# Optimization experiments

Hardware: AMD Instinct MI355X
Metric: run time of the kernel (lower is better)

Reference implementation:

```python
import jax, jax.numpy as jnp
import numpy as np

E_DIM = 640   # RNA-FM embedding dim
H = 256       # hidden_dim
L = 3         # num_gcn_layers
LN_EPS = 1e-5


def _layer_norm(x, g, b):
    mu = jnp.mean(x, axis=-1, keepdims=True)
    var = jnp.mean((x - mu) ** 2, axis=-1, keepdims=True)
    return (x - mu) * jax.lax.rsqrt(var + LN_EPS) * g + b


def setup_inputs() -> dict:
    key = jax.random.key(0)
    ks = jax.random.split(key, 20)
    B, S = 4, 256

    def w(k, shape):
        fan_in = shape[-2] if len(shape) >= 2 else shape[-1]
        return jax.random.normal(k, shape, dtype=jnp.float32) / np.sqrt(fan_in)

    inp = {
        "embeddings": jax.random.normal(ks[0], (B, S, E_DIM), dtype=jnp.float32),
        "bp_priors": jax.random.uniform(ks[1], (B, S, S), dtype=jnp.float32),
        "sequence_lengths": jnp.full((B,), S, dtype=jnp.int32),
        # FeatureEncoder: Linear(640, 512) -> ReLU -> Linear(512, 256)
        "enc_w1": w(ks[2], (E_DIM, 2 * H)), "enc_b1": jnp.zeros((2 * H,), jnp.float32),
        "enc_w2": w(ks[3], (2 * H, H)),     "enc_b2": jnp.zeros((H,), jnp.float32),
        # GCN layers (stacked over L)
        "gcn_wself": w(ks[4], (L, H, H)), "gcn_bself": jnp.zeros((L, H), jnp.float32),
        "gcn_wedge": w(ks[5], (L, H, H)), "gcn_bedge": jnp.zeros((L, H), jnp.float32),
        "gcn_ln_g": jnp.ones((L, H), jnp.float32), "gcn_ln_b": jnp.zeros((L, H), jnp.float32),
        # PairwiseScorer MLP: Linear(2H+1, H) -> ReLU -> Linear(H, H//2) -> ReLU -> Linear(H//2, 1)
        "mlp_w1": w(ks[6], (2 * H + 1, H)), "mlp_b1": jnp.zeros((H,), jnp.float32),
        "mlp_w2": w(ks[7], (H, H // 2)),    "mlp_b2": jnp.zeros((H // 2,), jnp.float32),
        "mlp_w3": w(ks[8], (H // 2, 1)),    "mlp_b3": jnp.zeros((1,), jnp.float32),
    }
    return inp


def reference(embeddings, bp_priors, sequence_lengths,
              enc_w1, enc_b1, enc_w2, enc_b2,
              gcn_wself, gcn_bself, gcn_wedge, gcn_bedge, gcn_ln_g, gcn_ln_b,
              mlp_w1, mlp_b1, mlp_w2, mlp_b2, mlp_w3, mlp_b3):
    # FeatureEncoder
    h = jax.nn.relu(embeddings @ enc_w1 + enc_b1) @ enc_w2 + enc_b2  # [B,S,H]

    # GCN layers: self GEMM + adjacency (bp_priors) aggregated neighbor GEMM
    for l in range(L):
        self_f = h @ gcn_wself[l] + gcn_bself[l]
        neigh_f = jnp.einsum('bij,bjh->bih', bp_priors, h @ gcn_wedge[l] + gcn_bedge[l])
        h = _layer_norm(jax.nn.relu(self_f + neigh_f), gcn_ln_g[l], gcn_ln_b[l])

    # PairwiseScorer: concat([node_i, node_j, prior]) @ W1 split into three partial products
    # (mathematically identical to the expand-concat-MLP in the torch module).
    hi = h @ mlp_w1[:H]           # [B,S,H] contribution of node_i
    hj = h @ mlp_w1[H:2 * H]      # [B,S,H] contribution of node_j
    p = jax.nn.relu(hi[:, :, None, :] + hj[:, None, :, :]
                    + bp_priors[..., None] * mlp_w1[2 * H] + mlp_b1)  # [B,S,S,H]
    p = jax.nn.relu(p @ mlp_w2 + mlp_b2)                              # [B,S,S,H//2]
    bp_scores = (p @ mlp_w3 + mlp_b3)[..., 0]                         # [B,S,S]
    return bp_scores
```

## Files before the change

### kernel.cpp

```cpp
#include <hip/hip_runtime.h>

typedef __attribute__((ext_vector_type(8))) short short8;
typedef __attribute__((ext_vector_type(4))) float f32x4;

__device__ __forceinline__ void gload_lds16(const void* g, void* l) {
    __builtin_amdgcn_global_load_lds(
        (const __attribute__((address_space(1))) unsigned*)g,
        (__attribute__((address_space(3))) unsigned*)l, 16, 0, 0);
}
#define MFMA16(a, b, c) __builtin_amdgcn_mfma_f32_16x16x32_bf16((a), (b), (c), 0, 0, 0)

__global__ __launch_bounds__(256)
void splitw2(const float* __restrict__ w2, short* __restrict__ w2th,
             short* __restrict__ w2tl)
{
    int e = blockIdx.x * 256 + threadIdx.x;
    int k = e >> 7, n = e & 127;
    float x = w2[e];
    unsigned hu = __float_as_uint(x) & 0xFFFF0000u;
    w2th[n * 256 + k] = (short)(hu >> 16);
    w2tl[n * 256 + k] = (short)(__float_as_uint(x - __uint_as_float(hu)) >> 16);
}

template<bool RELU, bool LNA>
__global__ __launch_bounds__(256)
void gemm_f32(const float* __restrict__ A,
              const float* __restrict__ B0, const float* __restrict__ bias0,
              float* __restrict__ C0,
              const float* __restrict__ B1, const float* __restrict__ bias1,
              float* __restrict__ C1,
              const float* __restrict__ ps, const float* __restrict__ lg,
              const float* __restrict__ lb,
              int M, int N, int K, int nxHalf)
{
    int bx = blockIdx.x;
    const float* B = B0; const float* bias = bias0; float* C = C0;
    if (nxHalf && bx >= nxHalf) { bx -= nxHalf; B = B1; bias = bias1; C = C1; }
    const int m0 = blockIdx.y * 32, n0 = bx * 64;
    const int tid = threadIdx.x;
    const int tx = tid & 15, ty = tid >> 4;

    __shared__ __align__(16) float As[32 * 36];
    __shared__ __align__(16) float Bs[32 * 68];
    __shared__ float mus[32], rss[32];

    if (LNA) {
        if (tid < 32) {
            int m = m0 + tid;
            float s  = ps[m * 2]            + ps[2048 + m * 2]
                     + ps[4096 + m * 2]     + ps[6144 + m * 2];
            float s2 = ps[m * 2 + 1]        + ps[2048 + m * 2 + 1]
                     + ps[4096 + m * 2 + 1] + ps[6144 + m * 2 + 1];
            float mu  = s * (1.f / 256.f);
            float var = s2 * (1.f / 256.f) - mu * mu;
            mus[tid] = mu;
            rss[tid] = rsqrtf(var + 1e-5f);
        }
        __syncthreads();
    }

    float acc[2][4] = {};
    for (int k0 = 0; k0 < K; k0 += 32) {
        {
            int row = tid >> 3, kq = (tid & 7) << 2;
            float4 v = *(const float4*)&A[(long)(m0 + row) * K + k0 + kq];
            if (LNA) {
                float4 gv = *(const float4*)&lg[k0 + kq];
                float4 bv = *(const float4*)&lb[k0 + kq];
                float mu = mus[row], rs = rss[row];
                v.x = (v.x - mu) * rs * gv.x + bv.x;
                v.y = (v.y - mu) * rs * gv.y + bv.y;
                v.z = (v.z - mu) * rs * gv.z + bv.z;
                v.w = (v.w - mu) * rs * gv.w + bv.w;
            }
            As[(kq + 0) * 36 + row] = v.x; As[(kq + 1) * 36 + row] = v.y;
            As[(kq + 2) * 36 + row] = v.z; As[(kq + 3) * 36 + row] = v.w;
        }
#pragma unroll
        for (int q = 0; q < 2; ++q) {
            int f = tid * 2 + q;
            int kk = f >> 4, nn = (f & 15) << 2;
            *(float4*)&Bs[kk * 68 + nn] = *(const float4*)&B[(long)(k0 + kk) * N + n0 + nn];
        }
        __syncthreads();
#pragma unroll
        for (int k = 0; k < 32; ++k) {
            float2 a2 = *(const float2*)&As[k * 36 + ty * 2];
            float4 b4 = *(const float4*)&Bs[k * 68 + tx * 4];
            acc[0][0] += a2.x * b4.x; acc[0][1] += a2.x * b4.y;
            acc[0][2] += a2.x * b4.z; acc[0][3] += a2.x * b4.w;
            acc[1][0] += a2.y * b4.x; acc[1][1] += a2.y * b4.y;
            acc[1][2] += a2.y * b4.z; acc[1][3] += a2.y * b4.w;
        }
        __syncthreads();
    }

#pragma unroll
    for (int i = 0; i < 2; ++i) {
        int m = m0 + ty * 2 + i;
#pragma unroll
        for (int j = 0; j < 4; ++j) {
            int n = n0 + tx * 4 + j;
            float v = acc[i][j];
            if (bias) v += bias[n];
            if (RELU) v = fmaxf(v, 0.f);
            C[(long)m * N + n] = v;
        }
    }
}

__global__ __launch_bounds__(256)
void bmm_fuse(const float* __restrict__ bp, const float* __restrict__ eg,
              const float* __restrict__ sf, float* __restrict__ x,
              float* __restrict__ ps)
{
    const int b = blockIdx.z, jb = blockIdx.x;
    const int m0 = blockIdx.y * 32, n0 = jb * 64;
    const float* A = bp + b * 65536;
    const float* B = eg + b * 65536;
    const int tid = threadIdx.x;
    const int tx = tid & 15, ty = tid >> 4;

    __shared__ __align__(16) float As[32 * 36];
    __shared__ __align__(16) float Bs[32 * 68];

    float acc[2][4] = {};
    for (int k0 = 0; k0 < 256; k0 += 32) {
        {
            int row = tid >> 3, kq = (tid & 7) << 2;
            float4 v = *(const float4*)&A[(long)(m0 + row) * 256 + k0 + kq];
            As[(kq + 0) * 36 + row] = v.x; As[(kq + 1) * 36 + row] = v.y;
            As[(kq + 2) * 36 + row] = v.z; As[(kq + 3) * 36 + row] = v.w;
        }
#pragma unroll
        for (int q = 0; q < 2; ++q) {
            int f = tid * 2 + q;
            int kk = f >> 4, nn = (f & 15) << 2;
            *(float4*)&Bs[kk * 68 + nn] = *(const float4*)&B[(long)(k0 + kk) * 256 + n0 + nn];
        }
        __syncthreads();
#pragma unroll
        for (int k = 0; k < 32; ++k) {
            float2 a2 = *(const float2*)&As[k * 36 + ty * 2];
            float4 b4 = *(const float4*)&Bs[k * 68 + tx * 4];
            acc[0][0] += a2.x * b4.x; acc[0][1] += a2.x * b4.y;
            acc[0][2] += a2.x * b4.z; acc[0][3] += a2.x * b4.w;
            acc[1][0] += a2.y * b4.x; acc[1][1] += a2.y * b4.y;
            acc[1][2] += a2.y * b4.z; acc[1][3] += a2.y * b4.w;
        }
        __syncthreads();
    }

#pragma unroll
    for (int i = 0; i < 2; ++i) {
        int gm = b * 256 + m0 + ty * 2 + i;
        float s = 0.f, s2 = 0.f;
#pragma unroll
        for (int j = 0; j < 4; ++j) {
            int n = n0 + tx * 4 + j;
            float v = fmaxf(acc[i][j] + sf[(long)gm * 256 + n], 0.f);
            x[(long)gm * 256 + n] = v;
            s += v; s2 += v * v;
        }
        s  += __shfl_xor(s, 1, 64);  s2 += __shfl_xor(s2, 1, 64);
        s  += __shfl_xor(s, 2, 64);  s2 += __shfl_xor(s2, 2, 64);
        s  += __shfl_xor(s, 4, 64);  s2 += __shfl_xor(s2, 4, 64);
        s  += __shfl_xor(s, 8, 64);  s2 += __shfl_xor(s2, 8, 64);
        if (tx == 0) {
            ps[jb * 2048 + gm * 2]     = s;
            ps[jb * 2048 + gm * 2 + 1] = s2;
        }
    }
}

#define STAGE_HJ(T, BUF)                                                        \
    {                                                                           \
        int row = tid >> 3, q = tid & 7;                                        \
        gload_lds16(&hja[((long)(b * 256 + j0 + row)) * 256 + (T) * 32          \
                         + (q ^ (row & 7)) * 4],                                \
                    (char*)&hjs[BUF][0] + tid * 16);                            \
        int row2 = row + 32;                                                    \
        gload_lds16(&hja[((long)(b * 256 + j0 + row2)) * 256 + (T) * 32         \
                         + (q ^ (row2 & 7)) * 4],                               \
                    (char*)&hjs[BUF][0] + 4096 + tid * 16);                     \
    }

#define BUILD_P(KT, BUF)                                                        \
    {                                                                           \
        const int p = tid >> 1, kb = (tid & 1) << 4;                            \
        const int ii = p >> 6, jj = p & 63;                                     \
        const float bw = bpv[p];                                                \
        const int swz = (p & 7) << 4;                                           \
        char* ph = (char*)&Ph[BUF][0];                                          \
        char* pl = (char*)&Pl[BUF][0];                                          \
        const char* hbase = (const char*)&hjs[BUF][0] + jj * 128;               \
        _Pragma("unroll")                                                       \
        for (int q = 0; q < 4; ++q) {                                           \
            int kk = kb + q * 4;                                                \
            float4 hv = *(const float4*)(hbase + ((((kk >> 2) ^ (jj & 7))) << 4)); \
            float4 iv = *(const float4*)&hib[ii][(KT) * 32 + kk];               \
            float4 cv = *(const float4*)&csv[(KT) * 32 + kk];                   \
            float x0 = fmaxf(iv.x + hv.x + bw * cv.x, 0.f);                     \
            float x1 = fmaxf(iv.y + hv.y + bw * cv.y, 0.f);                     \
            float x2 = fmaxf(iv.z + hv.z + bw * cv.z, 0.f);                     \
            float x3 = fmaxf(iv.w + hv.w + bw * cv.w, 0.f);                     \
            unsigned h0 = __float_as_uint(x0) & 0xFFFF0000u;                    \
            unsigned h1 = __float_as_uint(x1) & 0xFFFF0000u;                    \
            unsigned h2 = __float_as_uint(x2) & 0xFFFF0000u;                    \
            unsigned h3 = __float_as_uint(x3) & 0xFFFF0000u;                    \
            unsigned l0 = __float_as_uint(x0 - __uint_as_float(h0));            \
            unsigned l1 = __float_as_uint(x1 - __uint_as_float(h1));            \
            unsigned l2 = __float_as_uint(x2 - __uint_as_float(h2));            \
            unsigned l3 = __float_as_uint(x3 - __uint_as_float(h3));            \
            int bb2 = p * 64 + kk * 2;                                          \
            *(unsigned*)(ph + ((bb2    ) ^ swz)) = (h0 >> 16) | h1;             \
            *(unsigned*)(ph + ((bb2 + 4) ^ swz)) = (h2 >> 16) | h3;             \
            *(unsigned*)(pl + ((bb2    ) ^ swz)) = (l0 >> 16) | (l1 & 0xFFFF0000u); \
            *(unsigned*)(pl + ((bb2 + 4) ^ swz)) = (l2 >> 16) | (l3 & 0xFFFF0000u); \
        }                                                                       \
    }

__global__ __launch_bounds__(256, 3)
void pairwise3(const float* __restrict__ hia, const float* __restrict__ hja,
               const float* __restrict__ bpm,
               const float* __restrict__ c, const float* __restrict__ b1,
               const short* __restrict__ w2th, const short* __restrict__ w2tl,
               const float* __restrict__ b2, const float* __restrict__ w3,
               const float* __restrict__ b3, float* __restrict__ out)
{
    const int b = blockIdx.z, ib0 = blockIdx.y * 2, j0 = blockIdx.x * 64;
    const int tid = threadIdx.x, l = tid & 63, wid = tid >> 6;
    const int wm0 = (wid & 1) * 64, wn0 = (wid >> 1) * 64;
    const int g = l >> 4, ln = l & 15;

    __shared__ __align__(16) short Ph[2][4096];
    __shared__ __align__(16) short Pl[2][4096];
    __shared__ __align__(16) float hjs[2][2048];
    __shared__ __align__(16) float hib[2][256];
    __shared__ __align__(16) float csv[256];
    __shared__ float bpv[128];
    __shared__ float red[128][2];

    if (tid < 128)
        bpv[tid] = bpm[((long)(b * 256 + ib0 + (tid >> 6))) * 256 + j0 + (tid & 63)];
    {
        int i2 = tid >> 7, kk = (tid & 127) * 2;
        float2 hv = *(const float2*)&hia[((long)(b * 256 + ib0 + i2)) * 256 + kk];
        float2 bv = *(const float2*)&b1[kk];
        hib[i2][kk] = hv.x + bv.x; hib[i2][kk + 1] = hv.y + bv.y;
    }
    if (tid < 64) *(float4*)&csv[tid * 4] = *(const float4*)&c[tid * 4];

    STAGE_HJ(0, 0);
    __syncthreads();
    STAGE_HJ(1, 1);
    BUILD_P(0, 0);
    __syncthreads();

    f32x4 acc[4][4] = {};

#pragma unroll
    for (int kt = 0; kt < 8; ++kt) {
        const int cur = kt & 1;
        short8 bh[4], bl[4];
#pragma unroll
        for (int nf = 0; nf < 4; ++nf) {
            int col = wn0 + nf * 16 + ln;
            long bo = (long)col * 256 + kt * 32 + g * 8;
            bh[nf] = *(const short8*)(w2th + bo);
            bl[nf] = *(const short8*)(w2tl + bo);
        }
        short8 ah[4], al[4];
#pragma unroll
        for (int mf = 0; mf < 4; ++mf) {
            int row = wm0 + mf * 16 + ln;
            int off = (row * 64 + g * 16) ^ ((row & 7) << 4);
            ah[mf] = *(const short8*)((const char*)&Ph[cur][0] + off);
            al[mf] = *(const short8*)((const char*)&Pl[cur][0] + off);
        }
        if (kt < 6) STAGE_HJ(kt + 2, cur);
        if (kt < 7) BUILD_P(kt + 1, cur ^ 1);
#pragma unroll
        for (int mf = 0; mf < 4; ++mf)
#pragma unroll
            for (int nf = 0; nf < 4; ++nf) {
                acc[mf][nf] = MFMA16(ah[mf], bh[nf], acc[mf][nf]);
                acc[mf][nf] = MFMA16(ah[mf], bl[nf], acc[mf][nf]);
                acc[mf][nf] = MFMA16(al[mf], bh[nf], acc[mf][nf]);
            }
        __syncthreads();
    }

    float b2v[4], w3v[4];
#pragma unroll
    for (int nf = 0; nf < 4; ++nf) {
        int col = wn0 + nf * 16 + ln;
        b2v[nf] = b2[col];
        w3v[nf] = w3[col];
    }
#pragma unroll
    for (int mf = 0; mf < 4; ++mf) {
#pragma unroll
        for (int r = 0; r < 4; ++r) {
            float s = 0.f;
#pragma unroll
            for (int nf = 0; nf < 4; ++nf)
                s += fmaxf(acc[mf][nf][r] + b2v[nf], 0.f) * w3v[nf];
            s += __shfl_xor(s, 1, 64);
            s += __shfl_xor(s, 2, 64);
            s += __shfl_xor(s, 4, 64);
            s += __shfl_xor(s, 8, 64);
            if (ln == 0)
                red[wm0 + mf * 16 + g * 4 + r][wid >> 1] = s;
        }
    }
    __syncthreads();
    if (tid < 128) {
        int i = ib0 + (tid >> 6), j = j0 + (tid & 63);
        out[((long)(b * 256 + i)) * 256 + j] = red[tid][0] + red[tid][1] + b3[0];
    }
}

extern "C" void kernel_launch(void* const* d_in, const int* in_sizes, int n_in,
                              void* d_out, int out_size, void* d_ws, size_t ws_size,
                              hipStream_t stream)
{
    const float* emb   = (const float*)d_in[0];
    const float* bp    = (const float*)d_in[1];
    const float* ew1   = (const float*)d_in[3];
    const float* eb1   = (const float*)d_in[4];
    const float* ew2   = (const float*)d_in[5];
    const float* eb2   = (const float*)d_in[6];
    const float* wself = (const float*)d_in[7];
    const float* bself = (const float*)d_in[8];
    const float* wedge = (const float*)d_in[9];
    const float* bedge = (const float*)d_in[10];
    const float* lng   = (const float*)d_in[11];
    const float* lnb   = (const float*)d_in[12];
    const float* mw1   = (const float*)d_in[13];
    const float* mb1   = (const float*)d_in[14];
    const float* mw2   = (const float*)d_in[15];
    const float* mb2   = (const float*)d_in[16];
    const float* mw3   = (const float*)d_in[17];
    const float* mb3   = (const float*)d_in[18];
    float* out = (float*)d_out;

    float* ws = (float*)d_ws;
    float* h1 = ws;
    float* xe = h1 + 524288;
    float* sf = xe + 262144;
    float* eg = sf + 262144;
    float* x0 = eg + 262144;
    float* x1 = x0 + 262144;
    float* x2 = x1 + 262144;
    float* hi = x2 + 262144;
    float* hj = hi + 262144;
    short* w2th = (short*)(hj + 262144);
    short* w2tl = w2th + 32768;
    float* ps0  = (float*)(w2tl + 32768);
    float* ps1  = ps0 + 8192;
    float* ps2  = ps1 + 8192;

    float* xs[3]  = {x0, x1, x2};
    float* pss[3] = {ps0, ps1, ps2};
    dim3 blk(256);

    splitw2<<<dim3(128), blk, 0, stream>>>(mw2, w2th, w2tl);

    gemm_f32<true, false><<<dim3(8, 32), blk, 0, stream>>>(emb, ew1, eb1, h1,
        nullptr, nullptr, nullptr, nullptr, nullptr, nullptr, 1024, 512, 640, 0);
    gemm_f32<false, false><<<dim3(4, 32), blk, 0, stream>>>(h1, ew2, eb2, xe,
        nullptr, nullptr, nullptr, nullptr, nullptr, nullptr, 1024, 256, 512, 0);

    for (int l = 0; l < 3; ++l) {
        const float* Ain = (l == 0) ? xe : xs[l - 1];
        if (l == 0)
            gemm_f32<false, false><<<dim3(8, 32), blk, 0, stream>>>(Ain,
                wself, bself, sf, wedge, bedge, eg,
                nullptr, nullptr, nullptr, 1024, 256, 256, 4);
        else
            gemm_f32<false, true><<<dim3(8, 32), blk, 0, stream>>>(Ain,
                wself + l * 65536, bself + l * 256, sf,
                wedge + l * 65536, bedge + l * 256, eg,
                pss[l - 1], lng + (l - 1) * 256, lnb + (l - 1) * 256,
                1024, 256, 256, 4);
        bmm_fuse<<<dim3(4, 8, 4), blk, 0, stream>>>(bp, eg, sf, xs[l], pss[l]);
    }

    gemm_f32<false, true><<<dim3(8, 32), blk, 0, stream>>>(x2,
        mw1, nullptr, hi, mw1 + 65536, nullptr, hj,
        ps2, lng + 512, lnb + 512, 1024, 256, 256, 4);

    pairwise3<<<dim3(4, 128, 4), blk, 0, stream>>>(hi, hj, bp,
        mw1 + 131072, mb1, w2th, w2tl, mb2, mw3, mb3, out);
}
```

Measured before the change: 315.6 us.

## Shrink GEMM tiles, fold w2 split into encoder GEMM, vectorize pairwise P build

The fp32 GEMM kernel drops from a 32x64 to a 32x32 output tile per block, doubling the grid so more CUs are busy on these small matrices. The standalone splitw2 launch is merged into the first encoder GEMM as extra blocks, removing one launch. In the pairwise kernel, BUILD_P now handles 8 contiguous k values per thread and writes 16-byte stores instead of four 4-byte stores. The STAGE_HJ/BUILD_P calls are moved ahead of the A-fragment LDS reads to change the overlap with the MFMAs. Smaller tiles cut per-thread reuse and raise load traffic per FLOP in the GEMMs.

```diff
diff --git a/kernel.cpp b/kernel.cpp
--- a/kernel.cpp
+++ b/kernel.cpp
@@ -2,6 +2,7 @@
 
 typedef __attribute__((ext_vector_type(8))) short short8;
 typedef __attribute__((ext_vector_type(4))) float f32x4;
+typedef __attribute__((ext_vector_type(4))) unsigned uint4v;
 
 __device__ __forceinline__ void gload_lds16(const void* g, void* l) {
     __builtin_amdgcn_global_load_lds(
@@ -10,38 +11,39 @@
 }
 #define MFMA16(a, b, c) __builtin_amdgcn_mfma_f32_16x16x32_bf16((a), (b), (c), 0, 0, 0)
 
+template<bool RELU, bool LNA, bool SPLITW2>
 __global__ __launch_bounds__(256)
-void splitw2(const float* __restrict__ w2, short* __restrict__ w2th,
-             short* __restrict__ w2tl)
+void gemm_s(const float* __restrict__ A,
+            const float* __restrict__ B0, const float* __restrict__ bias0,
+            float* __restrict__ C0,
+            const float* __restrict__ B1, const float* __restrict__ bias1,
+            float* __restrict__ C1,
+            const float* __restrict__ ps, const float* __restrict__ lg,
+            const float* __restrict__ lb,
+            int M, int N, int K, int nxHalf,
+            const float* __restrict__ w2, short* __restrict__ w2th,
+            short* __restrict__ w2tl)
 {
-    int e = blockIdx.x * 256 + threadIdx.x;
-    int k = e >> 7, n = e & 127;
-    float x = w2[e];
-    unsigned hu = __float_as_uint(x) & 0xFFFF0000u;
-    w2th[n * 256 + k] = (short)(hu >> 16);
-    w2tl[n * 256 + k] = (short)(__float_as_uint(x - __uint_as_float(hu)) >> 16);
-}
-
-template<bool RELU, bool LNA>
-__global__ __launch_bounds__(256)
-void gemm_f32(const float* __restrict__ A,
-              const float* __restrict__ B0, const float* __restrict__ bias0,
-              float* __restrict__ C0,
-              const float* __restrict__ B1, const float* __restrict__ bias1,
-              float* __restrict__ C1,
-              const float* __restrict__ ps, const float* __restrict__ lg,
-              const float* __restrict__ lb,
-              int M, int N, int K, int nxHalf)
-{
+    if (SPLITW2 && blockIdx.y >= 32) {
+        int e = ((blockIdx.y - 32) * gridDim.x + blockIdx.x) * 256 + threadIdx.x;
+        if (e < 32768) {
+            int k = e >> 7, n = e & 127;
+            float x = w2[e];
+            unsigned hu = __float_as_uint(x) & 0xFFFF0000u;
+            w2th[n * 256 + k] = (short)(hu >> 16);
+            w2tl[n * 256 + k] = (short)(__float_as_uint(x - __uint_as_float(hu)) >> 16);
+        }
+        return;
+    }
     int bx = blockIdx.x;
     const float* B = B0; const float* bias = bias0; float* C = C0;
     if (nxHalf && bx >= nxHalf) { bx -= nxHalf; B = B1; bias = bias1; C = C1; }
-    const int m0 = blockIdx.y * 32, n0 = bx * 64;
+    const int m0 = blockIdx.y * 32, n0 = bx * 32;
     const int tid = threadIdx.x;
-    const int tx = tid & 15, ty = tid >> 4;
+    const int tx = tid & 7, ty = tid >> 3;
 
     __shared__ __align__(16) float As[32 * 36];
-    __shared__ __align__(16) float Bs[32 * 68];
+    __shared__ __align__(16) float Bs[32 * 36];
     __shared__ float mus[32], rss[32];
 
     if (LNA) {
@@ -59,10 +61,10 @@
         __syncthreads();
     }
 
-    float acc[2][4] = {};
+    float acc[4] = {};
     for (int k0 = 0; k0 < K; k0 += 32) {
         {
-            int row = tid >> 3, kq = (tid & 7) << 2;
+            int row = ty, kq = tx << 2;
             float4 v = *(const float4*)&A[(long)(m0 + row) * K + k0 + kq];
             if (LNA) {
                 float4 gv = *(const float4*)&lg[k0 + kq];
@@ -76,36 +78,27 @@
             As[(kq + 0) * 36 + row] = v.x; As[(kq + 1) * 36 + row] = v.y;
             As[(kq + 2) * 36 + row] = v.z; As[(kq + 3) * 36 + row] = v.w;
         }
-#pragma unroll
-        for (int q = 0; q < 2; ++q) {
-            int f = tid * 2 + q;
-            int kk = f >> 4, nn = (f & 15) << 2;
-            *(float4*)&Bs[kk * 68 + nn] = *(const float4*)&B[(long)(k0 + kk) * N + n0 + nn];
-        }
+        *(float4*)&Bs[ty * 36 + tx * 4] =
+            *(const float4*)&B[(long)(k0 + ty) * N + n0 + tx * 4];
         __syncthreads();
 #pragma unroll
         for (int k = 0; k < 32; ++k) {
-            float2 a2 = *(const float2*)&As[k * 36 + ty * 2];
-            float4 b4 = *(const float4*)&Bs[k * 68 + tx * 4];
-            acc[0][0] += a2.x * b4.x; acc[0][1] += a2.x * b4.y;
-            acc[0][2] += a2.x * b4.z; acc[0][3] += a2.x * b4.w;
-            acc[1][0] += a2.y * b4.x; acc[1][1] += a2.y * b4.y;
-            acc[1][2] += a2.y * b4.z; acc[1][3] += a2.y * b4.w;
-        }
-        __syncthreads();
-    }
-
-#pragma unroll
-    for (int i = 0; i < 2; ++i) {
-        int m = m0 + ty * 2 + i;
-#pragma unroll
-        for (int j = 0; j < 4; ++j) {
-            int n = n0 + tx * 4 + j;
-            float v = acc[i][j];
-            if (bias) v += bias[n];
-            if (RELU) v = fmaxf(v, 0.f);
-            C[(long)m * N + n] = v;
-        }
+            float a = As[k * 36 + ty];
+            float4 b4 = *(const float4*)&Bs[k * 36 + tx * 4];
+            acc[0] += a * b4.x; acc[1] += a * b4.y;
+            acc[2] += a * b4.z; acc[3] += a * b4.w;
+        }
+        __syncthreads();
+    }
+
+    int m = m0 + ty;
+#pragma unroll
+    for (int j = 0; j < 4; ++j) {
+        int n = n0 + tx * 4 + j;
+        float v = acc[j];
+        if (bias) v += bias[n];
+        if (RELU) v = fmaxf(v, 0.f);
+        C[(long)m * N + n] = v;
     }
 }
 
@@ -175,53 +168,68 @@
 
 #define STAGE_HJ(T, BUF)                                                        \
     {                                                                           \
-        int row = tid >> 3, q = tid & 7;                                        \
+        int row = tid >> 3, s = tid & 7;                                        \
         gload_lds16(&hja[((long)(b * 256 + j0 + row)) * 256 + (T) * 32          \
-                         + (q ^ (row & 7)) * 4],                                \
+                         + ((s ^ (row & 7)) << 2)],                             \
                     (char*)&hjs[BUF][0] + tid * 16);                            \
         int row2 = row + 32;                                                    \
         gload_lds16(&hja[((long)(b * 256 + j0 + row2)) * 256 + (T) * 32         \
-                         + (q ^ (row2 & 7)) * 4],                               \
+                         + ((s ^ (row2 & 7)) << 2)],                            \
                     (char*)&hjs[BUF][0] + 4096 + tid * 16);                     \
     }
 
 #define BUILD_P(KT, BUF)                                                        \
     {                                                                           \
-        const int p = tid >> 1, kb = (tid & 1) << 4;                            \
-        const int ii = p >> 6, jj = p & 63;                                     \
-        const float bw = bpv[p];                                                \
+        const char* hbase = (const char*)&hjs[BUF][0] + jj * 128;               \
+        char* phc = (char*)&Ph[BUF][0];                                         \
+        char* plc = (char*)&Pl[BUF][0];                                         \
         const int swz = (p & 7) << 4;                                           \
-        char* ph = (char*)&Ph[BUF][0];                                          \
-        char* pl = (char*)&Pl[BUF][0];                                          \
-        const char* hbase = (const char*)&hjs[BUF][0] + jj * 128;               \
         _Pragma("unroll")                                                       \
-        for (int q = 0; q < 4; ++q) {                                           \
-            int kk = kb + q * 4;                                                \
-            float4 hv = *(const float4*)(hbase + ((((kk >> 2) ^ (jj & 7))) << 4)); \
-            float4 iv = *(const float4*)&hib[ii][(KT) * 32 + kk];               \
-            float4 cv = *(const float4*)&csv[(KT) * 32 + kk];                   \
-            float x0 = fmaxf(iv.x + hv.x + bw * cv.x, 0.f);                     \
-            float x1 = fmaxf(iv.y + hv.y + bw * cv.y, 0.f);                     \
-            float x2 = fmaxf(iv.z + hv.z + bw * cv.z, 0.f);                     \
-            float x3 = fmaxf(iv.w + hv.w + bw * cv.w, 0.f);                     \
+        for (int q = 0; q < 2; ++q) {                                           \
+            const int oct = o0 + q;                                             \
+            float4 hv0 = *(const float4*)(hbase + (((oct * 2)     ^ (jj & 7)) << 4)); \
+            float4 hv1 = *(const float4*)(hbase + (((oct * 2 + 1) ^ (jj & 7)) << 4)); \
+            float4 iv0 = *(const float4*)&hib[ii][(KT) * 32 + oct * 8];         \
+            float4 iv1 = *(const float4*)&hib[ii][(KT) * 32 + oct * 8 + 4];     \
+            float4 cv0 = *(const float4*)&csv[(KT) * 32 + oct * 8];             \
+            float4 cv1 = *(const float4*)&csv[(KT) * 32 + oct * 8 + 4];         \
+            float x0 = fmaxf(fmaf(bpw, cv0.x, iv0.x) + hv0.x, 0.f);             \
+            float x1 = fmaxf(fmaf(bpw, cv0.y, iv0.y) + hv0.y, 0.f);             \
+            float x2 = fmaxf(fmaf(bpw, cv0.z, iv0.z) + hv0.z, 0.f);             \
+            float x3 = fmaxf(fmaf(bpw, cv0.w, iv0.w) + hv0.w, 0.f);             \
+            float x4 = fmaxf(fmaf(bpw, cv1.x, iv1.x) + hv1.x, 0.f);             \
+            float x5 = fmaxf(fmaf(bpw, cv1.y, iv1.y) + hv1.y, 0.f);             \
+            float x6 = fmaxf(fmaf(bpw, cv1.z, iv1.z) + hv1.z, 0.f);             \
+            float x7 = fmaxf(fmaf(bpw, cv1.w, iv1.w) + hv1.w, 0.f);             \
             unsigned h0 = __float_as_uint(x0) & 0xFFFF0000u;                    \
             unsigned h1 = __float_as_uint(x1) & 0xFFFF0000u;                    \
             unsigned h2 = __float_as_uint(x2) & 0xFFFF0000u;                    \
             unsigned h3 = __float_as_uint(x3) & 0xFFFF0000u;                    \
-            unsigned l0 = __float_as_uint(x0 - __uint_as_float(h0));            \
-            unsigned l1 = __float_as_uint(x1 - __uint_as_float(h1));            \
-            unsigned l2 = __float_as_uint(x2 - __uint_as_float(h2));            \
-            unsigned l3 = __float_as_uint(x3 - __uint_as_float(h3));            \
-            int bb2 = p * 64 + kk * 2;                                          \
-            *(unsigned*)(ph + ((bb2    ) ^ swz)) = (h0 >> 16) | h1;             \
-            *(unsigned*)(ph + ((bb2 + 4) ^ swz)) = (h2 >> 16) | h3;             \
-            *(unsigned*)(pl + ((bb2    ) ^ swz)) = (l0 >> 16) | (l1 & 0xFFFF0000u); \
-            *(unsigned*)(pl + ((bb2 + 4) ^ swz)) = (l2 >> 16) | (l3 & 0xFFFF0000u); \
+            unsigned h4 = __float_as_uint(x4) & 0xFFFF0000u;                    \
+            unsigned h5 = __float_as_uint(x5) & 0xFFFF0000u;                    \
+            unsigned h6 = __float_as_uint(x6) & 0xFFFF0000u;                    \
+            unsigned h7 = __float_as_uint(x7) & 0xFFFF0000u;                    \
+            uint4v hv_, lv_;                                                    \
+            hv_[0] = (h0 >> 16) | h1;                                           \
+            hv_[1] = (h2 >> 16) | h3;                                           \
+            hv_[2] = (h4 >> 16) | h5;                                           \
+            hv_[3] = (h6 >> 16) | h7;                                           \
+            lv_[0] = (__float_as_uint(x0 - __uint_as_float(h0)) >> 16)          \
+                   | (__float_as_uint(x1 - __uint_as_float(h1)) & 0xFFFF0000u); \
+            lv_[1] = (__float_as_uint(x2 - __uint_as_float(h2)) >> 16)          \
+                   | (__float_as_uint(x3 - __uint_as_float(h3)) & 0xFFFF0000u); \
+            lv_[2] = (__float_as_uint(x4 - __uint_as_float(h4)) >> 16)          \
+                   | (__float_as_uint(x5 - __uint_as_float(h5)) & 0xFFFF0000u); \
+            lv_[3] = (__float_as_uint(x6 - __uint_as_float(h6)) >> 16)          \
+                   | (__float_as_uint(x7 - __uint_as_float(h7)) & 0xFFFF0000u); \
+            int sbyte = p * 64 + oct * 16;                                      \
+            *(uint4v*)(phc + (sbyte ^ swz)) = hv_;                              \
+            *(uint4v*)(plc + (sbyte ^ swz)) = lv_;                              \
         }                                                                       \
     }
 
 __global__ __launch_bounds__(256, 3)
-void pairwise3(const float* __restrict__ hia, const float* __restrict__ hja,
+void pairwise4(const float* __restrict__ hia, const float* __restrict__ hja,
                const float* __restrict__ bpm,
                const float* __restrict__ c, const float* __restrict__ b1,
                const short* __restrict__ w2th, const short* __restrict__ w2tl,
@@ -232,6 +240,7 @@
     const int tid = threadIdx.x, l = tid & 63, wid = tid >> 6;
     const int wm0 = (wid & 1) * 64, wn0 = (wid >> 1) * 64;
     const int g = l >> 4, ln = l & 15;
+    const int p = tid >> 1, jj = p & 63, ii = p >> 6, o0 = (tid & 1) * 2;
 
     __shared__ __align__(16) short Ph[2][4096];
     __shared__ __align__(16) short Pl[2][4096];
@@ -253,6 +262,7 @@
 
     STAGE_HJ(0, 0);
     __syncthreads();
+    const float bpw = bpv[p];
     STAGE_HJ(1, 1);
     BUILD_P(0, 0);
     __syncthreads();
@@ -262,6 +272,7 @@
 #pragma unroll
     for (int kt = 0; kt < 8; ++kt) {
         const int cur = kt & 1;
+        if (kt < 6) STAGE_HJ(kt + 2, cur);
         short8 bh[4], bl[4];
 #pragma unroll
         for (int nf = 0; nf < 4; ++nf) {
@@ -270,6 +281,7 @@
             bh[nf] = *(const short8*)(w2th + bo);
             bl[nf] = *(const short8*)(w2tl + bo);
         }
+        if (kt < 7) BUILD_P(kt + 1, cur ^ 1);
         short8 ah[4], al[4];
 #pragma unroll
         for (int mf = 0; mf < 4; ++mf) {
@@ -278,8 +290,6 @@
             ah[mf] = *(const short8*)((const char*)&Ph[cur][0] + off);
             al[mf] = *(const short8*)((const char*)&Pl[cur][0] + off);
         }
-        if (kt < 6) STAGE_HJ(kt + 2, cur);
-        if (kt < 7) BUILD_P(kt + 1, cur ^ 1);
 #pragma unroll
         for (int mf = 0; mf < 4; ++mf)
 #pragma unroll
@@ -365,32 +375,34 @@
     float* pss[3] = {ps0, ps1, ps2};
     dim3 blk(256);
 
-    splitw2<<<dim3(128), blk, 0, stream>>>(mw2, w2th, w2tl);
-
-    gemm_f32<true, false><<<dim3(8, 32), blk, 0, stream>>>(emb, ew1, eb1, h1,
-        nullptr, nullptr, nullptr, nullptr, nullptr, nullptr, 1024, 512, 640, 0);
-    gemm_f32<false, false><<<dim3(4, 32), blk, 0, stream>>>(h1, ew2, eb2, xe,
-        nullptr, nullptr, nullptr, nullptr, nullptr, nullptr, 1024, 256, 512, 0);
-
-    for (int l = 0; l < 3; ++l) {
-        const float* Ain = (l == 0) ? xe : xs[l - 1];
-        if (l == 0)
-            gemm_f32<false, false><<<dim3(8, 32), blk, 0, stream>>>(Ain,
+    gemm_s<true, false, true><<<dim3(16, 40), blk, 0, stream>>>(emb, ew1, eb1, h1,
+        nullptr, nullptr, nullptr, nullptr, nullptr, nullptr,
+        1024, 512, 640, 0, mw2, w2th, w2tl);
+    gemm_s<false, false, false><<<dim3(8, 32), blk, 0, stream>>>(h1, ew2, eb2, xe,
+        nullptr, nullptr, nullptr, nullptr, nullptr, nullptr,
+        1024, 256, 512, 0, nullptr, nullptr, nullptr);
+
+    for (int lyr = 0; lyr < 3; ++lyr) {
+        const float* Ain = (lyr == 0) ? xe : xs[lyr - 1];
+        if (lyr == 0)
+            gemm_s<false, false, false><<<dim3(16, 32), blk, 0, stream>>>(Ain,
                 wself, bself, sf, wedge, bedge, eg,
-                nullptr, nullptr, nullptr, 1024, 256, 256, 4);
+                nullptr, nullptr, nullptr, 1024, 256, 256, 8,
+                nullptr, nullptr, nullptr);
         else
-            gemm_f32<false, true><<<dim3(8, 32), blk, 0, stream>>>(Ain,
-                wself + l * 65536, bself + l * 256, sf,
-                wedge + l * 65536, bedge + l * 256, eg,
-                pss[l - 1], lng + (l - 1) * 256, lnb + (l - 1) * 256,
-                1024, 256, 256, 4);
-        bmm_fuse<<<dim3(4, 8, 4), blk, 0, stream>>>(bp, eg, sf, xs[l], pss[l]);
-    }
-
-    gemm_f32<false, true><<<dim3(8, 32), blk, 0, stream>>>(x2,
+            gemm_s<false, true, false><<<dim3(16, 32), blk, 0, stream>>>(Ain,
+                wself + lyr * 65536, bself + lyr * 256, sf,
+                wedge + lyr * 65536, bedge + lyr * 256, eg,
+                pss[lyr - 1], lng + (lyr - 1) * 256, lnb + (lyr - 1) * 256,
+                1024, 256, 256, 8, nullptr, nullptr, nullptr);
+        bmm_fuse<<<dim3(4, 8, 4), blk, 0, stream>>>(bp, eg, sf, xs[lyr], pss[lyr]);
+    }
+
+    gemm_s<false, true, false><<<dim3(16, 32), blk, 0, stream>>>(x2,
         mw1, nullptr, hi, mw1 + 65536, nullptr, hj,
-        ps2, lng + 512, lnb + 512, 1024, 256, 256, 4);
-
-    pairwise3<<<dim3(4, 128, 4), blk, 0, stream>>>(hi, hj, bp,
+        ps2, lng + 512, lnb + 512, 1024, 256, 256, 8,
+        nullptr, nullptr, nullptr);
+
+    pairwise4<<<dim3(4, 128, 4), blk, 0, stream>>>(hi, hj, bp,
         mw1 + 131072, mb1, w2th, w2tl, mb2, mw3, mb3, out);
 }
```

Result: faster. 303.0 us (-4.0%).
